# Optimization experiments

Measured on AMD Instinct MI355X. Metric: run time of the kernel, lower is better.

Reference implementation:

```python
import jax, jax.numpy as jnp
import numpy as np

B, T, C, H = 8, 2048, 1024, 64

def setup_inputs() -> dict:
    key = jax.random.key(0)
    k1, k2, k3, k4 = jax.random.split(key, 4)
    x = jax.random.normal(k1, (B, T, C), dtype=jnp.float32)
    sw = 1.0 / np.sqrt(C)  # Linear-like init scale
    Wq = jax.random.normal(k2, (C, H), dtype=jnp.float32) * sw
    Wk = jax.random.normal(k3, (C, H), dtype=jnp.float32) * sw
    Wv = jax.random.normal(k4, (C, H), dtype=jnp.float32) * sw
    return {"x": x, "Wq": Wq, "Wk": Wk, "Wv": Wv}

def reference(x, Wq, Wk, Wv):
    # Single-head causal self-attention (eval mode: dropout is identity).
    # Quantized GEMMs (QLinear / qmatmul) are represented by exact fp32 math.
    Bx, Tx, Cx = x.shape
    q = jnp.einsum('btc,ch->bth', x, Wq)          # [B,T,H]
    k = jnp.einsum('btc,ch->bth', x, Wk)          # [B,T,H]
    v = jnp.einsum('btc,ch->bth', x, Wv)          # [B,T,H]
    scale = k.shape[-1] ** -0.5
    wei = jnp.einsum('bth,bsh->bts', q, k) * scale  # [B,T,T]
    causal = jnp.tril(jnp.ones((Tx, Tx), dtype=bool))
    wei = jnp.where(causal, wei, -jnp.inf)
    wei = jax.nn.softmax(wei, axis=-1)
    out = jnp.einsum('bts,bsh->bth', wei, v)      # [B,T,H]
    return out
```

## Files before the change

### kernel.cpp

```cpp
#include <hip/hip_runtime.h>
#include <math.h>

#define Bz 8
#define Tz 2048
#define Cz 1024
#define Hz 64
#define BT (Bz*Tz)

typedef __attribute__((ext_vector_type(8))) short bf16x8;
typedef __attribute__((ext_vector_type(4))) float f32x4;
typedef __attribute__((ext_vector_type(4))) unsigned short us4;

#define PSTRIDE 4160

__device__ __forceinline__ unsigned short f2bf(float f) {
    union { float f; unsigned u; } v; v.f = f;
    unsigned r = v.u + 0x7fffu + ((v.u >> 16) & 1u);
    return (unsigned short)(r >> 16);
}

__device__ __forceinline__ bf16x8 pack8(const float* s) {
    bf16x8 r;
#pragma unroll
    for (int j = 0; j < 8; j++) r[j] = (short)f2bf(s[j]);
    return r;
}

__device__ __forceinline__ void gload16(const void* g, void* l) {
    __builtin_amdgcn_global_load_lds(
        (const __attribute__((address_space(1))) void*)g,
        (__attribute__((address_space(3))) void*)l, 16, 0, 0);
}

__global__ __launch_bounds__(256)
void wprep_kernel(const float* __restrict__ Wq, const float* __restrict__ Wk,
                  const float* __restrict__ Wv, unsigned short* __restrict__ Wt)
{
    __shared__ float T[64][65];
    const int mat = blockIdx.x >> 4;
    const int k0  = (blockIdx.x & 15) * 64;
    const float* W = (mat == 0) ? Wq : (mat == 1) ? Wk : Wv;
    const int t  = threadIdx.x;
    const int rr = t >> 2;
    const int c4 = (t & 3) * 16;
#pragma unroll
    for (int j = 0; j < 4; j++) {
        float4 w4 = *(const float4*)&W[(size_t)(k0 + rr) * Hz + c4 + j * 4];
        T[c4 + j*4 + 0][rr] = w4.x;
        T[c4 + j*4 + 1][rr] = w4.y;
        T[c4 + j*4 + 2][rr] = w4.z;
        T[c4 + j*4 + 3][rr] = w4.w;
    }
    __syncthreads();
    const int nn = t >> 2;
    const int ks = (t & 3) * 16;
    float tmp[16];
#pragma unroll
    for (int j = 0; j < 16; j++) tmp[j] = T[nn][ks + j];
    unsigned short* dst = &Wt[(size_t)(mat * 64 + nn) * Cz + k0 + ks];
    *(bf16x8*)dst       = pack8(tmp);
    *(bf16x8*)(dst + 8) = pack8(tmp + 8);
}

__global__ __launch_bounds__(256, 2)
void qkv_mfma_kernel(const float* __restrict__ x, const unsigned short* __restrict__ Wt,
                     unsigned short* __restrict__ qg, unsigned short* __restrict__ kg,
                     unsigned short* __restrict__ vT)
{
    __shared__ unsigned short xs[32 * 64];
    __shared__ unsigned short ws[192 * 64];

    const int t  = threadIdx.x;
    const int M0 = blockIdx.x * 32;
    const int ln = t & 15;
    const int g  = (t & 63) >> 4;
    const int g4 = g * 4;
    const int w  = t >> 6;
    const int wr = w & 1;
    const int wc = w >> 1;
    const float SCq = 0.18033688011112042f;

    f32x4 acc[6];
#pragma unroll
    for (int i = 0; i < 6; i++) acc[i] = (f32x4){0.f, 0.f, 0.f, 0.f};

    const int xrow = t >> 3;
    const int xsl  = t & 7;
    int wn[6], wsl[6];
#pragma unroll
    for (int i = 0; i < 6; i++) {
        const int c = i * 256 + t;
        wn[i] = c >> 3; wsl[i] = c & 7;
    }

    float4 xf0, xf1;
    bf16x8 wreg[6];

    auto load_chunk = [&](int k0) {
        const float* src = &x[(size_t)(M0 + xrow) * Cz + k0 + xsl * 8];
        xf0 = *(const float4*)src;
        xf1 = *(const float4*)(src + 4);
#pragma unroll
        for (int i = 0; i < 6; i++)
            wreg[i] = *(const bf16x8*)&Wt[(size_t)wn[i] * Cz + k0 + wsl[i] * 8];
    };
    auto write_chunk = [&]() {
        float tmp[8];
        tmp[0]=xf0.x; tmp[1]=xf0.y; tmp[2]=xf0.z; tmp[3]=xf0.w;
        tmp[4]=xf1.x; tmp[5]=xf1.y; tmp[6]=xf1.z; tmp[7]=xf1.w;
        *(bf16x8*)&xs[xrow*64 + (xsl ^ (xrow & 7)) * 8] = pack8(tmp);
#pragma unroll
        for (int i = 0; i < 6; i++)
            *(bf16x8*)&ws[wn[i]*64 + (wsl[i] ^ (wn[i] & 7)) * 8] = wreg[i];
    };

    load_chunk(0);
    write_chunk();
    for (int kt = 0; kt < 16; kt++) {
        __syncthreads();
        if (kt < 15) load_chunk((kt + 1) * 64);

        bf16x8 af[2];
        const int m = wr * 16 + ln;
#pragma unroll
        for (int kc = 0; kc < 2; kc++)
            af[kc] = *(const bf16x8*)&xs[m*64 + ((kc*4 + g) ^ (m & 7)) * 8];
        __builtin_amdgcn_s_setprio(1);
#pragma unroll
        for (int ct = 0; ct < 6; ct++) {
            const int nn = wc * 96 + ct * 16 + ln;
#pragma unroll
            for (int kc = 0; kc < 2; kc++) {
                bf16x8 bf = *(const bf16x8*)&ws[nn*64 + ((kc*4 + g) ^ (nn & 7)) * 8];
                acc[ct] = __builtin_amdgcn_mfma_f32_16x16x32_bf16(af[kc], bf, acc[ct], 0, 0, 0);
            }
        }
        __builtin_amdgcn_s_setprio(0);
        __syncthreads();
        if (kt < 15) write_chunk();
    }

#pragma unroll
    for (int ct = 0; ct < 6; ct++) {
        const int col0 = wc * 96 + ct * 16;
        const int mat  = col0 >> 6;
        const int cl   = (col0 & 63) + ln;
        const int m0   = M0 + wr * 16 + g4;
        if (mat == 0) {
#pragma unroll
            for (int i = 0; i < 4; i++)
                qg[(size_t)(m0 + i) * Hz + cl] = f2bf(acc[ct][i] * SCq);
        } else if (mat == 1) {
#pragma unroll
            for (int i = 0; i < 4; i++)
                kg[(size_t)(m0 + i) * Hz + cl] = f2bf(acc[ct][i]);
        } else {
            const int b = m0 >> 11, tt = m0 & 2047;
            us4 pk;
#pragma unroll
            for (int i = 0; i < 4; i++) pk[i] = f2bf(acc[ct][i]);
            *(us4*)&vT[((size_t)b * Hz + cl) * Tz + tt] = pk;
        }
    }
}

template<int S>
__global__ __launch_bounds__(256, 4)
void attn_mfma_kernel(const unsigned short* __restrict__ qg,
                      const unsigned short* __restrict__ kg,
                      const unsigned short* __restrict__ vT,
                      float* __restrict__ pbase)
{
    __shared__ unsigned short Ks [2][64 * 64];
    __shared__ unsigned short Vts[2][64 * 64];
    __shared__ unsigned short Ps [4 * 16 * 64];

    const int bid  = blockIdx.x;
    const int c    = bid % S;
    const int tmp0 = bid / S;
    const int b    = tmp0 & 7;
    const int qt   = 31 - (tmp0 >> 3);
    if (c > qt) return;
    const int q0   = qt * 64;

    const int t  = threadIdx.x;
    const int ln = t & 15;
    const int g  = (t & 63) >> 4;
    const int g4 = g * 4;
    const int w  = t >> 6;
    const int l6 = t & 63;

    const unsigned short* qb = qg + (size_t)b * Tz * Hz;
    const unsigned short* kb = kg + (size_t)b * Tz * Hz;
    const unsigned short* vb = vT + (size_t)b * Hz * Tz;

    bf16x8 qf[2];
    {
        const int qrow = q0 + w*16 + ln;
        qf[0] = *(const bf16x8*)&qb[(size_t)qrow * Hz + g*8];
        qf[1] = *(const bf16x8*)&qb[(size_t)qrow * Hz + 32 + g*8];
    }

    const int rl  = l6 >> 3;
    const int swz = ((l6 & 7) ^ rl) * 8;
    auto issue_tile = [&](int buf, int s0) {
#pragma unroll
        for (int qq = 0; qq < 2; qq++) {
            const int row = w*16 + qq*8 + rl;
            gload16(&kb[(size_t)(s0 + row) * Hz + swz],
                    &Ks[buf][(w*16 + qq*8) * 64]);
            gload16(&vb[(size_t)row * Tz + s0 + swz],
                    &Vts[buf][(w*16 + qq*8) * 64]);
        }
    };

    f32x4 accO[4];
#pragma unroll
    for (int i = 0; i < 4; i++) accO[i] = (f32x4){0.f, 0.f, 0.f, 0.f};
    float lrow[4] = {0.f, 0.f, 0.f, 0.f};

    unsigned short* Pw = &Ps[w * 1024];

    issue_tile(0, c * 64);
    __syncthreads();
    int cur = 0;

    for (int s = c; s <= qt; s += S) {
        if (s + S <= qt) issue_tile(cur ^ 1, (s + S) * 64);

        const unsigned short* Kc = &Ks[cur][0];
        const unsigned short* Vc = &Vts[cur][0];

        f32x4 accS[4];
        __builtin_amdgcn_s_setprio(1);
#pragma unroll
        for (int t4 = 0; t4 < 4; t4++) {
            accS[t4] = (f32x4){0.f, 0.f, 0.f, 0.f};
#pragma unroll
            for (int kc = 0; kc < 2; kc++) {
                const int n = t4*16 + ln;
                bf16x8 kf = *(const bf16x8*)&Kc[n*64 + ((kc*4 + g) ^ (n & 7)) * 8];
                accS[t4] = __builtin_amdgcn_mfma_f32_16x16x32_bf16(qf[kc], kf, accS[t4], 0, 0, 0);
            }
        }
        __builtin_amdgcn_s_setprio(0);

        const bool diag = (s == qt);
#pragma unroll
        for (int t4 = 0; t4 < 4; t4++) {
#pragma unroll
            for (int i = 0; i < 4; i++) {
                float sv = accS[t4][i];
                if (diag && (t4*16 + ln > w*16 + g4 + i)) sv = -1e30f;
                const float p = exp2f(sv);
                lrow[i] += p;
                const int col = t4*16 + ln;
                const int row = g4 + i;
                Pw[row*64 + ((col >> 3) ^ (row & 7)) * 8 + (col & 7)] = f2bf(p);
            }
        }

        __builtin_amdgcn_s_setprio(1);
#pragma unroll
        for (int kc = 0; kc < 2; kc++) {
            bf16x8 pa = *(const bf16x8*)&Pw[ln*64 + ((kc*4 + g) ^ (ln & 7)) * 8];
#pragma unroll
            for (int ht = 0; ht < 4; ht++) {
                const int vr2 = ht*16 + ln;
                bf16x8 vf = *(const bf16x8*)&Vc[vr2*64 + ((kc*4 + g) ^ (vr2 & 7)) * 8];
                accO[ht] = __builtin_amdgcn_mfma_f32_16x16x32_bf16(pa, vf, accO[ht], 0, 0, 0);
            }
        }
        __builtin_amdgcn_s_setprio(0);

        __syncthreads();
        cur ^= 1;
    }

#pragma unroll
    for (int i = 0; i < 4; i++) {
#pragma unroll
        for (int d = 1; d < 16; d <<= 1)
            lrow[i] += __shfl_xor(lrow[i], d);
    }
    float* Op = pbase + (size_t)((b * 32 + qt) * S + c) * PSTRIDE;
#pragma unroll
    for (int ht = 0; ht < 4; ht++)
#pragma unroll
        for (int i = 0; i < 4; i++)
            Op[(size_t)(w*16 + g4 + i) * 64 + ht*16 + ln] = accO[ht][i];
    if (ln == 0) {
#pragma unroll
        for (int i = 0; i < 4; i++)
            Op[4096 + w*16 + g4 + i] = lrow[i];
    }
}

template<int S>
__global__ __launch_bounds__(256)
void combine_kernel(const float* __restrict__ pbase, float* __restrict__ out)
{
    const int bid = blockIdx.x;
    const int b   = bid >> 5;
    const int qt  = bid & 31;
    const int t   = threadIdx.x;
    const int r   = t >> 2;
    const int cg  = t & 3;

    const int nch = (qt + 1 < S) ? (qt + 1) : S;
    const float* P0 = pbase + (size_t)(b * 32 + qt) * S * PSTRIDE;

    float denom = 0.f;
    float4 o[4];
#pragma unroll
    for (int j = 0; j < 4; j++) o[j] = make_float4(0.f, 0.f, 0.f, 0.f);
    for (int cc = 0; cc < nch; cc++) {
        const float* Pc = P0 + (size_t)cc * PSTRIDE;
        denom += Pc[4096 + r];
#pragma unroll
        for (int j = 0; j < 4; j++) {
            float4 v4 = *(const float4*)&Pc[(size_t)r * 64 + cg * 16 + j * 4];
            o[j].x += v4.x; o[j].y += v4.y; o[j].z += v4.z; o[j].w += v4.w;
        }
    }
    const float inv = 1.f / denom;
    float* ob = out + ((size_t)b * Tz + qt * 64 + r) * Hz + cg * 16;
#pragma unroll
    for (int j = 0; j < 4; j++)
        *(float4*)&ob[j * 4] = make_float4(o[j].x * inv, o[j].y * inv,
                                           o[j].z * inv, o[j].w * inv);
}

extern "C" void kernel_launch(void* const* d_in, const int* in_sizes, int n_in,
                              void* d_out, int out_size, void* d_ws, size_t ws_size,
                              hipStream_t stream) {
    const float* x  = (const float*)d_in[0];
    const float* Wq = (const float*)d_in[1];
    const float* Wk = (const float*)d_in[2];
    const float* Wv = (const float*)d_in[3];

    unsigned short* Wt = (unsigned short*)d_ws;
    unsigned short* qg = Wt + 196608;
    unsigned short* kg = qg + (size_t)BT * Hz;
    unsigned short* vT = kg + (size_t)BT * Hz;
    const size_t baseShorts = 196608 + 3 * (size_t)BT * Hz;
    float* pbase = (float*)((char*)d_ws + baseShorts * 2);
    float* out = (float*)d_out;

    wprep_kernel<<<48, 256, 0, stream>>>(Wq, Wk, Wv, Wt);
    qkv_mfma_kernel<<<BT / 32, 256, 0, stream>>>(x, Wt, qg, kg, vT);

    const size_t base = baseShorts * 2;
    const size_t per  = (size_t)8 * 32 * PSTRIDE * 4;
    if (ws_size >= base + 8 * per) {
        attn_mfma_kernel<8><<<8 * 32 * 8, 256, 0, stream>>>(qg, kg, vT, pbase);
        combine_kernel<8><<<256, 256, 0, stream>>>(pbase, out);
    } else if (ws_size >= base + 4 * per) {
        attn_mfma_kernel<4><<<8 * 32 * 4, 256, 0, stream>>>(qg, kg, vT, pbase);
        combine_kernel<4><<<256, 256, 0, stream>>>(pbase, out);
    } else {
        attn_mfma_kernel<1><<<8 * 32 * 1, 256, 0, stream>>>(qg, kg, vT, pbase);
        combine_kernel<1><<<256, 256, 0, stream>>>(pbase, out);
    }
}
```

Measured before the change: 52.16 us.

## Fuse split-K combine into attention and stream QKV tiles via LDS DMA

Replaces the split-across-blocks attention and its separate combine kernel with a single 512-thread kernel per query tile. Two wave groups process alternating key tiles and reduce their partial outputs through shared memory before writing the normalized result, which removes the partial-buffer round trip and one launch. The QKV projection now uses 64-row blocks with double-buffered direct global-to-LDS loads of fp32 x and of pre-swizzled bf16 weights, converting x to bf16 at fragment-read time. The trade-off is fewer attention blocks (256) with only two-way key parallelism, which may leave the device underfilled and makes the long causal tiles dominate.

```diff
diff --git a/kernel.cpp b/kernel.cpp
--- a/kernel.cpp
+++ b/kernel.cpp
@@ -11,8 +11,6 @@
 typedef __attribute__((ext_vector_type(4))) float f32x4;
 typedef __attribute__((ext_vector_type(4))) unsigned short us4;
 
-#define PSTRIDE 4160
-
 __device__ __forceinline__ unsigned short f2bf(float f) {
     union { float f; unsigned u; } v; v.f = f;
     unsigned r = v.u + 0x7fffu + ((v.u >> 16) & 1u);
@@ -26,6 +24,15 @@
     return r;
 }
 
+__device__ __forceinline__ bf16x8 pack8f4(float4 a, float4 b) {
+    bf16x8 r;
+    r[0] = (short)f2bf(a.x); r[1] = (short)f2bf(a.y);
+    r[2] = (short)f2bf(a.z); r[3] = (short)f2bf(a.w);
+    r[4] = (short)f2bf(b.x); r[5] = (short)f2bf(b.y);
+    r[6] = (short)f2bf(b.z); r[7] = (short)f2bf(b.w);
+    return r;
+}
+
 __device__ __forceinline__ void gload16(const void* g, void* l) {
     __builtin_amdgcn_global_load_lds(
         (const __attribute__((address_space(1))) void*)g,
@@ -34,11 +41,12 @@
 
 __global__ __launch_bounds__(256)
 void wprep_kernel(const float* __restrict__ Wq, const float* __restrict__ Wk,
-                  const float* __restrict__ Wv, unsigned short* __restrict__ Wt)
+                  const float* __restrict__ Wv, unsigned short* __restrict__ Wti)
 {
     __shared__ float T[64][65];
     const int mat = blockIdx.x >> 4;
-    const int k0  = (blockIdx.x & 15) * 64;
+    const int kt  = blockIdx.x & 15;
+    const int k0  = kt * 64;
     const float* W = (mat == 0) ? Wq : (mat == 1) ? Wk : Wv;
     const int t  = threadIdx.x;
     const int rr = t >> 2;
@@ -52,92 +60,86 @@
         T[c4 + j*4 + 3][rr] = w4.w;
     }
     __syncthreads();
-    const int nn = t >> 2;
-    const int ks = (t & 3) * 16;
+    const int nn  = t >> 2;
+    const int sl0 = (t & 3) * 2;
+    const int n   = mat * 64 + nn;
     float tmp[16];
 #pragma unroll
-    for (int j = 0; j < 16; j++) tmp[j] = T[nn][ks + j];
-    unsigned short* dst = &Wt[(size_t)(mat * 64 + nn) * Cz + k0 + ks];
-    *(bf16x8*)dst       = pack8(tmp);
-    *(bf16x8*)(dst + 8) = pack8(tmp + 8);
-}
-
-__global__ __launch_bounds__(256, 2)
-void qkv_mfma_kernel(const float* __restrict__ x, const unsigned short* __restrict__ Wt,
+    for (int j = 0; j < 16; j++) tmp[j] = T[nn][sl0 * 8 + j];
+    unsigned short* base = &Wti[(size_t)kt * 12288 + n * 64];
+    *(bf16x8*)&base[((sl0    ) ^ (n & 7)) * 8] = pack8(tmp);
+    *(bf16x8*)&base[((sl0 + 1) ^ (n & 7)) * 8] = pack8(tmp + 8);
+}
+
+__global__ __launch_bounds__(512, 2)
+void qkv_mfma_kernel(const float* __restrict__ x, const unsigned short* __restrict__ Wti,
                      unsigned short* __restrict__ qg, unsigned short* __restrict__ kg,
                      unsigned short* __restrict__ vT)
 {
-    __shared__ unsigned short xs[32 * 64];
-    __shared__ unsigned short ws[192 * 64];
-
-    const int t  = threadIdx.x;
-    const int M0 = blockIdx.x * 32;
-    const int ln = t & 15;
-    const int g  = (t & 63) >> 4;
-    const int g4 = g * 4;
-    const int w  = t >> 6;
-    const int wr = w & 1;
-    const int wc = w >> 1;
+    __shared__ __align__(16) float          xsF[2][64 * 64];
+    __shared__ __align__(16) unsigned short ws [2][192 * 64];
+
+    const int t    = threadIdx.x;
+    const int M0   = blockIdx.x * 64;
+    const int ln   = t & 15;
+    const int g    = (t & 63) >> 4;
+    const int g4   = g * 4;
+    const int w    = t >> 6;
+    const int rg   = w & 3;
+    const int wc   = w >> 2;
+    const int lane = t & 63;
     const float SCq = 0.18033688011112042f;
 
     f32x4 acc[6];
 #pragma unroll
     for (int i = 0; i < 6; i++) acc[i] = (f32x4){0.f, 0.f, 0.f, 0.f};
 
-    const int xrow = t >> 3;
-    const int xsl  = t & 7;
-    int wn[6], wsl[6];
-#pragma unroll
-    for (int i = 0; i < 6; i++) {
-        const int c = i * 256 + t;
-        wn[i] = c >> 3; wsl[i] = c & 7;
-    }
-
-    float4 xf0, xf1;
-    bf16x8 wreg[6];
-
-    auto load_chunk = [&](int k0) {
-        const float* src = &x[(size_t)(M0 + xrow) * Cz + k0 + xsl * 8];
-        xf0 = *(const float4*)src;
-        xf1 = *(const float4*)(src + 4);
-#pragma unroll
-        for (int i = 0; i < 6; i++)
-            wreg[i] = *(const bf16x8*)&Wt[(size_t)wn[i] * Cz + k0 + wsl[i] * 8];
+    auto issue = [&](int buf, int kt) {
+        const int k0 = kt * 64;
+#pragma unroll
+        for (int j = 0; j < 2; j++) {
+            const int r  = w * 8 + j * 4 + (lane >> 4);
+            const int sl = (lane & 15) ^ (r & 7);
+            gload16(&x[(size_t)(M0 + r) * Cz + k0 + sl * 4],
+                    &xsF[buf][(w * 8 + j * 4) * 64]);
+        }
+#pragma unroll
+        for (int j = 0; j < 3; j++) {
+            const int jj = w * 3 + j;
+            gload16(&Wti[(size_t)kt * 12288 + jj * 512 + lane * 8],
+                    &ws[buf][jj * 512]);
+        }
     };
-    auto write_chunk = [&]() {
-        float tmp[8];
-        tmp[0]=xf0.x; tmp[1]=xf0.y; tmp[2]=xf0.z; tmp[3]=xf0.w;
-        tmp[4]=xf1.x; tmp[5]=xf1.y; tmp[6]=xf1.z; tmp[7]=xf1.w;
-        *(bf16x8*)&xs[xrow*64 + (xsl ^ (xrow & 7)) * 8] = pack8(tmp);
-#pragma unroll
-        for (int i = 0; i < 6; i++)
-            *(bf16x8*)&ws[wn[i]*64 + (wsl[i] ^ (wn[i] & 7)) * 8] = wreg[i];
-    };
-
-    load_chunk(0);
-    write_chunk();
+
+    issue(0, 0);
+    __syncthreads();
+    int cur = 0;
+
     for (int kt = 0; kt < 16; kt++) {
-        __syncthreads();
-        if (kt < 15) load_chunk((kt + 1) * 64);
+        if (kt < 15) issue(cur ^ 1, kt + 1);
 
         bf16x8 af[2];
-        const int m = wr * 16 + ln;
-#pragma unroll
-        for (int kc = 0; kc < 2; kc++)
-            af[kc] = *(const bf16x8*)&xs[m*64 + ((kc*4 + g) ^ (m & 7)) * 8];
+        const int row = rg * 16 + ln;
+#pragma unroll
+        for (int kc = 0; kc < 2; kc++) {
+            const int s0 = kc * 8 + g * 2;
+            float4 fa = *(const float4*)&xsF[cur][row * 64 + ((s0    ) ^ (row & 7)) * 4];
+            float4 fb = *(const float4*)&xsF[cur][row * 64 + ((s0 + 1) ^ (row & 7)) * 4];
+            af[kc] = pack8f4(fa, fb);
+        }
         __builtin_amdgcn_s_setprio(1);
 #pragma unroll
         for (int ct = 0; ct < 6; ct++) {
             const int nn = wc * 96 + ct * 16 + ln;
 #pragma unroll
             for (int kc = 0; kc < 2; kc++) {
-                bf16x8 bf = *(const bf16x8*)&ws[nn*64 + ((kc*4 + g) ^ (nn & 7)) * 8];
+                bf16x8 bf = *(const bf16x8*)&ws[cur][nn * 64 + ((kc*4 + g) ^ (nn & 7)) * 8];
                 acc[ct] = __builtin_amdgcn_mfma_f32_16x16x32_bf16(af[kc], bf, acc[ct], 0, 0, 0);
             }
         }
         __builtin_amdgcn_s_setprio(0);
         __syncthreads();
-        if (kt < 15) write_chunk();
+        cur ^= 1;
     }
 
 #pragma unroll
@@ -145,7 +147,7 @@
         const int col0 = wc * 96 + ct * 16;
         const int mat  = col0 >> 6;
         const int cl   = (col0 & 63) + ln;
-        const int m0   = M0 + wr * 16 + g4;
+        const int m0   = M0 + rg * 16 + g4;
         if (mat == 0) {
 #pragma unroll
             for (int i = 0; i < 4; i++)
@@ -164,30 +166,28 @@
     }
 }
 
-template<int S>
-__global__ __launch_bounds__(256, 4)
-void attn_mfma_kernel(const unsigned short* __restrict__ qg,
-                      const unsigned short* __restrict__ kg,
-                      const unsigned short* __restrict__ vT,
-                      float* __restrict__ pbase)
+__global__ __launch_bounds__(512, 2)
+void attn2_kernel(const unsigned short* __restrict__ qg,
+                  const unsigned short* __restrict__ kg,
+                  const unsigned short* __restrict__ vT,
+                  float* __restrict__ out)
 {
-    __shared__ unsigned short Ks [2][64 * 64];
-    __shared__ unsigned short Vts[2][64 * 64];
-    __shared__ unsigned short Ps [4 * 16 * 64];
-
-    const int bid  = blockIdx.x;
-    const int c    = bid % S;
-    const int tmp0 = bid / S;
-    const int b    = tmp0 & 7;
-    const int qt   = 31 - (tmp0 >> 3);
-    if (c > qt) return;
-    const int q0   = qt * 64;
+    __shared__ __align__(16) unsigned short Ks [2][2][64 * 64];
+    __shared__ __align__(16) unsigned short Vts[2][2][64 * 64];
+    __shared__ __align__(16) unsigned short Ps [8][16 * 64];
+
+    const int bid = blockIdx.x;
+    const int b   = bid & 7;
+    const int qt  = 31 - (bid >> 3);
+    const int q0  = qt * 64;
 
     const int t  = threadIdx.x;
     const int ln = t & 15;
     const int g  = (t & 63) >> 4;
     const int g4 = g * 4;
     const int w  = t >> 6;
+    const int wl = w & 3;
+    const int sc = w >> 2;
     const int l6 = t & 63;
 
     const unsigned short* qb = qg + (size_t)b * Tz * Hz;
@@ -196,9 +196,9 @@
 
     bf16x8 qf[2];
     {
-        const int qrow = q0 + w*16 + ln;
-        qf[0] = *(const bf16x8*)&qb[(size_t)qrow * Hz + g*8];
-        qf[1] = *(const bf16x8*)&qb[(size_t)qrow * Hz + 32 + g*8];
+        const int qrow = q0 + wl * 16 + ln;
+        qf[0] = *(const bf16x8*)&qb[(size_t)qrow * Hz + g * 8];
+        qf[1] = *(const bf16x8*)&qb[(size_t)qrow * Hz + 32 + g * 8];
     }
 
     const int rl  = l6 >> 3;
@@ -206,11 +206,11 @@
     auto issue_tile = [&](int buf, int s0) {
 #pragma unroll
         for (int qq = 0; qq < 2; qq++) {
-            const int row = w*16 + qq*8 + rl;
+            const int row = wl * 16 + qq * 8 + rl;
             gload16(&kb[(size_t)(s0 + row) * Hz + swz],
-                    &Ks[buf][(w*16 + qq*8) * 64]);
+                    &Ks[sc][buf][(wl * 16 + qq * 8) * 64]);
             gload16(&vb[(size_t)row * Tz + s0 + swz],
-                    &Vts[buf][(w*16 + qq*8) * 64]);
+                    &Vts[sc][buf][(wl * 16 + qq * 8) * 64]);
         }
     };
 
@@ -218,60 +218,66 @@
 #pragma unroll
     for (int i = 0; i < 4; i++) accO[i] = (f32x4){0.f, 0.f, 0.f, 0.f};
     float lrow[4] = {0.f, 0.f, 0.f, 0.f};
-
-    unsigned short* Pw = &Ps[w * 1024];
-
-    issue_tile(0, c * 64);
+    unsigned short* Pw = Ps[w];
+
+    const int n_mine = (qt >= sc) ? ((qt - sc) >> 1) + 1 : 0;
+    const int iters  = (qt >> 1) + 1;
+
+    if (n_mine > 0) issue_tile(0, sc * 64);
     __syncthreads();
     int cur = 0;
 
-    for (int s = c; s <= qt; s += S) {
-        if (s + S <= qt) issue_tile(cur ^ 1, (s + S) * 64);
-
-        const unsigned short* Kc = &Ks[cur][0];
-        const unsigned short* Vc = &Vts[cur][0];
-
-        f32x4 accS[4];
-        __builtin_amdgcn_s_setprio(1);
-#pragma unroll
-        for (int t4 = 0; t4 < 4; t4++) {
-            accS[t4] = (f32x4){0.f, 0.f, 0.f, 0.f};
+    for (int it = 0; it < iters; it++) {
+        const int s = sc + 2 * it;
+        const bool active = (it < n_mine);
+        if (active && (it + 1 < n_mine)) issue_tile(cur ^ 1, (s + 2) * 64);
+
+        if (active) {
+            const unsigned short* Kc = Ks[sc][cur];
+            const unsigned short* Vc = Vts[sc][cur];
+
+            f32x4 accS[4];
+            __builtin_amdgcn_s_setprio(1);
+#pragma unroll
+            for (int t4 = 0; t4 < 4; t4++) {
+                accS[t4] = (f32x4){0.f, 0.f, 0.f, 0.f};
+#pragma unroll
+                for (int kc = 0; kc < 2; kc++) {
+                    const int n = t4 * 16 + ln;
+                    bf16x8 kf = *(const bf16x8*)&Kc[n * 64 + ((kc*4 + g) ^ (n & 7)) * 8];
+                    accS[t4] = __builtin_amdgcn_mfma_f32_16x16x32_bf16(qf[kc], kf, accS[t4], 0, 0, 0);
+                }
+            }
+            __builtin_amdgcn_s_setprio(0);
+
+            const bool diag = (s == qt);
+#pragma unroll
+            for (int t4 = 0; t4 < 4; t4++) {
+#pragma unroll
+                for (int i = 0; i < 4; i++) {
+                    float sv = accS[t4][i];
+                    if (diag && (t4 * 16 + ln > wl * 16 + g4 + i)) sv = -1e30f;
+                    const float p = exp2f(sv);
+                    lrow[i] += p;
+                    const int col = t4 * 16 + ln;
+                    const int row = g4 + i;
+                    Pw[row * 64 + ((col >> 3) ^ (row & 7)) * 8 + (col & 7)] = f2bf(p);
+                }
+            }
+
+            __builtin_amdgcn_s_setprio(1);
 #pragma unroll
             for (int kc = 0; kc < 2; kc++) {
-                const int n = t4*16 + ln;
-                bf16x8 kf = *(const bf16x8*)&Kc[n*64 + ((kc*4 + g) ^ (n & 7)) * 8];
-                accS[t4] = __builtin_amdgcn_mfma_f32_16x16x32_bf16(qf[kc], kf, accS[t4], 0, 0, 0);
-            }
-        }
-        __builtin_amdgcn_s_setprio(0);
-
-        const bool diag = (s == qt);
-#pragma unroll
-        for (int t4 = 0; t4 < 4; t4++) {
-#pragma unroll
-            for (int i = 0; i < 4; i++) {
-                float sv = accS[t4][i];
-                if (diag && (t4*16 + ln > w*16 + g4 + i)) sv = -1e30f;
-                const float p = exp2f(sv);
-                lrow[i] += p;
-                const int col = t4*16 + ln;
-                const int row = g4 + i;
-                Pw[row*64 + ((col >> 3) ^ (row & 7)) * 8 + (col & 7)] = f2bf(p);
-            }
-        }
-
-        __builtin_amdgcn_s_setprio(1);
-#pragma unroll
-        for (int kc = 0; kc < 2; kc++) {
-            bf16x8 pa = *(const bf16x8*)&Pw[ln*64 + ((kc*4 + g) ^ (ln & 7)) * 8];
-#pragma unroll
-            for (int ht = 0; ht < 4; ht++) {
-                const int vr2 = ht*16 + ln;
-                bf16x8 vf = *(const bf16x8*)&Vc[vr2*64 + ((kc*4 + g) ^ (vr2 & 7)) * 8];
-                accO[ht] = __builtin_amdgcn_mfma_f32_16x16x32_bf16(pa, vf, accO[ht], 0, 0, 0);
-            }
-        }
-        __builtin_amdgcn_s_setprio(0);
+                bf16x8 pa = *(const bf16x8*)&Pw[ln * 64 + ((kc*4 + g) ^ (ln & 7)) * 8];
+#pragma unroll
+                for (int ht = 0; ht < 4; ht++) {
+                    const int vr2 = ht * 16 + ln;
+                    bf16x8 vf = *(const bf16x8*)&Vc[vr2 * 64 + ((kc*4 + g) ^ (vr2 & 7)) * 8];
+                    accO[ht] = __builtin_amdgcn_mfma_f32_16x16x32_bf16(pa, vf, accO[ht], 0, 0, 0);
+                }
+            }
+            __builtin_amdgcn_s_setprio(0);
+        }
 
         __syncthreads();
         cur ^= 1;
@@ -283,52 +289,37 @@
         for (int d = 1; d < 16; d <<= 1)
             lrow[i] += __shfl_xor(lrow[i], d);
     }
-    float* Op = pbase + (size_t)((b * 32 + qt) * S + c) * PSTRIDE;
-#pragma unroll
-    for (int ht = 0; ht < 4; ht++)
+
+    float* O1 = (float*)&Ks[0][0][0];
+    float* L1 = (float*)&Vts[0][0][0];
+    if (sc == 1) {
+#pragma unroll
+        for (int ht = 0; ht < 4; ht++)
+#pragma unroll
+            for (int i = 0; i < 4; i++)
+                O1[(wl * 16 + g4 + i) * 64 + ht * 16 + ln] = accO[ht][i];
+        if (ln == 0) {
+#pragma unroll
+            for (int i = 0; i < 4; i++)
+                L1[wl * 16 + g4 + i] = lrow[i];
+        }
+    }
+    __syncthreads();
+    if (sc == 0) {
+        float inv[4];
 #pragma unroll
         for (int i = 0; i < 4; i++)
-            Op[(size_t)(w*16 + g4 + i) * 64 + ht*16 + ln] = accO[ht][i];
-    if (ln == 0) {
-#pragma unroll
-        for (int i = 0; i < 4; i++)
-            Op[4096 + w*16 + g4 + i] = lrow[i];
-    }
-}
-
-template<int S>
-__global__ __launch_bounds__(256)
-void combine_kernel(const float* __restrict__ pbase, float* __restrict__ out)
-{
-    const int bid = blockIdx.x;
-    const int b   = bid >> 5;
-    const int qt  = bid & 31;
-    const int t   = threadIdx.x;
-    const int r   = t >> 2;
-    const int cg  = t & 3;
-
-    const int nch = (qt + 1 < S) ? (qt + 1) : S;
-    const float* P0 = pbase + (size_t)(b * 32 + qt) * S * PSTRIDE;
-
-    float denom = 0.f;
-    float4 o[4];
-#pragma unroll
-    for (int j = 0; j < 4; j++) o[j] = make_float4(0.f, 0.f, 0.f, 0.f);
-    for (int cc = 0; cc < nch; cc++) {
-        const float* Pc = P0 + (size_t)cc * PSTRIDE;
-        denom += Pc[4096 + r];
-#pragma unroll
-        for (int j = 0; j < 4; j++) {
-            float4 v4 = *(const float4*)&Pc[(size_t)r * 64 + cg * 16 + j * 4];
-            o[j].x += v4.x; o[j].y += v4.y; o[j].z += v4.z; o[j].w += v4.w;
-        }
-    }
-    const float inv = 1.f / denom;
-    float* ob = out + ((size_t)b * Tz + qt * 64 + r) * Hz + cg * 16;
-#pragma unroll
-    for (int j = 0; j < 4; j++)
-        *(float4*)&ob[j * 4] = make_float4(o[j].x * inv, o[j].y * inv,
-                                           o[j].z * inv, o[j].w * inv);
+            inv[i] = 1.f / (lrow[i] + L1[wl * 16 + g4 + i]);
+        float* ob = out + ((size_t)b * Tz + q0) * Hz;
+#pragma unroll
+        for (int ht = 0; ht < 4; ht++)
+#pragma unroll
+            for (int i = 0; i < 4; i++) {
+                const int r = wl * 16 + g4 + i;
+                ob[(size_t)r * Hz + ht * 16 + ln] =
+                    (accO[ht][i] + O1[r * 64 + ht * 16 + ln]) * inv[i];
+            }
+    }
 }
 
 extern "C" void kernel_launch(void* const* d_in, const int* in_sizes, int n_in,
@@ -339,27 +330,13 @@
     const float* Wk = (const float*)d_in[2];
     const float* Wv = (const float*)d_in[3];
 
-    unsigned short* Wt = (unsigned short*)d_ws;
-    unsigned short* qg = Wt + 196608;
-    unsigned short* kg = qg + (size_t)BT * Hz;
-    unsigned short* vT = kg + (size_t)BT * Hz;
-    const size_t baseShorts = 196608 + 3 * (size_t)BT * Hz;
-    float* pbase = (float*)((char*)d_ws + baseShorts * 2);
+    unsigned short* Wti = (unsigned short*)d_ws;
+    unsigned short* qg  = Wti + 196608;
+    unsigned short* kg  = qg + (size_t)BT * Hz;
+    unsigned short* vT  = kg + (size_t)BT * Hz;
     float* out = (float*)d_out;
 
-    wprep_kernel<<<48, 256, 0, stream>>>(Wq, Wk, Wv, Wt);
-    qkv_mfma_kernel<<<BT / 32, 256, 0, stream>>>(x, Wt, qg, kg, vT);
-
-    const size_t base = baseShorts * 2;
-    const size_t per  = (size_t)8 * 32 * PSTRIDE * 4;
-    if (ws_size >= base + 8 * per) {
-        attn_mfma_kernel<8><<<8 * 32 * 8, 256, 0, stream>>>(qg, kg, vT, pbase);
-        combine_kernel<8><<<256, 256, 0, stream>>>(pbase, out);
-    } else if (ws_size >= base + 4 * per) {
-        attn_mfma_kernel<4><<<8 * 32 * 4, 256, 0, stream>>>(qg, kg, vT, pbase);
-        combine_kernel<4><<<256, 256, 0, stream>>>(pbase, out);
-    } else {
-        attn_mfma_kernel<1><<<8 * 32 * 1, 256, 0, stream>>>(qg, kg, vT, pbase);
-        combine_kernel<1><<<256, 256, 0, stream>>>(pbase, out);
-    }
-}
+    wprep_kernel<<<48, 256, 0, stream>>>(Wq, Wk, Wv, Wti);
+    qkv_mfma_kernel<<<BT / 64, 512, 0, stream>>>(x, Wti, qg, kg, vT);
+    attn2_kernel<<<Bz * 32, 512, 0, stream>>>(qg, kg, vT, out);
+}
```

Result: slower. 60.95 us (+16.9%).
